# Optimization experiments

Measured on AMD Instinct MI355X. Metric: run time of the kernel, lower is better.

## Reference

```python
import jax, jax.numpy as jnp
import numpy as np
from jax import lax

B, V, E = 8, 1024, 32          # batch, nodes, raw node-embedding dim
F, H = 64, 4                   # node_encoding, num_heads
HID = 64                       # encoder/decoder hidden size
LAYERS = 2                     # graph_layers
FLOW_ITERS = 10
BIG = 1e9
COST_C = 1.0                   # quadratic cost: c*x^2, inv_derivative(y)=y/(2c)
DEG_P = 16.0 / V               # ~16 avg out-degree


def setup_inputs() -> dict:
    key = jax.random.key(0)
    ks = jax.random.split(key, 24)
    demands = jax.random.normal(ks[0], (B, V, 1), jnp.float32)
    demands = demands - jnp.mean(demands, axis=1, keepdims=True)  # balanced supply/demand
    node_embeddings = jax.random.normal(ks[1], (V, E), jnp.float32)
    adj = (jax.random.uniform(ks[2], (V, V)) < DEG_P).astype(jnp.float32)
    adj = jnp.maximum(adj, jnp.eye(V, dtype=jnp.float32))  # ensure nonempty rows
    s = 0.05
    p = lambda k, shp: jax.random.normal(k, shp, jnp.float32) * s
    return {
        'demands': demands, 'node_embeddings': node_embeddings, 'adj': adj,
        'enc_w1': p(ks[3], (E + 1, HID)), 'enc_b1': jnp.zeros((HID,), jnp.float32),
        'enc_w2': p(ks[4], (HID, F)),     'enc_b2': jnp.zeros((F,), jnp.float32),
        'gat_w':  p(ks[5], (H, F, F)),
        'gat_a1': p(ks[6], (H, F)), 'gat_a2': p(ks[7], (H, F)),
        'gate_w': p(ks[8], (F, F)), 'gate_u': p(ks[9], (F, F)),
        'gate_b': jnp.zeros((F,), jnp.float32),
        'dec_w1': p(ks[10], (F, HID)), 'dec_b1': jnp.zeros((HID,), jnp.float32),
        'dec_w2': p(ks[11], (HID, V)), 'dec_b2': jnp.zeros((V,), jnp.float32),
        'dual_w1': p(ks[12], (F, HID)), 'dual_b1': jnp.zeros((HID,), jnp.float32),
        'dual_w2': p(ks[13], (HID, 1)), 'dual_b2': jnp.zeros((1,), jnp.float32),
    }


def _forward(demands, node_embeddings, adj,
             enc_w1, enc_b1, enc_w2, enc_b2,
             gat_w, gat_a1, gat_a2,
             gate_w, gate_u, gate_b,
             dec_w1, dec_b1, dec_w2, dec_b2,
             dual_w1, dual_b1, dual_w2, dual_b2):
    node_bias = -BIG * (1.0 - adj)                     # [V, V]
    # ---- encoder MLP (relu hidden) ----
    x = jnp.broadcast_to(node_embeddings[None], (B, V, E))
    x = jnp.concatenate([x, demands], axis=2)          # [B, V, E+1]
    enc = jax.nn.relu(x @ enc_w1 + enc_b1) @ enc_w2 + enc_b2   # [B, V, F]
    enc = jax.nn.relu(enc)
    # ---- GAT + gate, shared weights across graph_layers ----
    for _ in range(LAYERS):
        t = jnp.einsum('bvf,hfg->bhvg', enc, gat_w)            # [B, H, V, F]
        s_self = jnp.einsum('bhvg,hg->bhv', t, gat_a1)
        s_nbr = jnp.einsum('bhvg,hg->bhv', t, gat_a2)
        logits = jax.nn.leaky_relu(s_self[..., :, None] + s_nbr[..., None, :], 0.2)
        coefs = jax.nn.softmax(logits + node_bias[None, None], axis=-1)  # [B,H,V,V]
        heads = jnp.einsum('bhvw,bhwg->bhvg', coefs, t)
        nxt = jax.nn.relu(jnp.mean(heads, axis=1))             # [B, V, F]
        z = jax.nn.sigmoid(nxt @ gate_w + enc @ gate_u + gate_b)
        enc = z * nxt + (1.0 - z) * enc
    # ---- decoder -> masked softmax flow weights ----
    pred = (enc @ dec_w1 + dec_b1) @ dec_w2 + dec_b2           # [B, V, V] (linear MLP)
    pred = jnp.square(pred)
    flow_weights = jax.nn.softmax(pred + node_bias[None], axis=-1)
    # ---- iterative min-cost-flow solve ----
    def flow_step(flow, _):
        inflow = jnp.sum(flow, axis=1)[:, :, None]             # [B, V, 1]
        return flow_weights * jax.nn.relu(inflow - demands), None
    flow, _ = lax.scan(flow_step, jnp.zeros_like(flow_weights), None, length=FLOW_ITERS)[0], None
    flow = lax.scan(flow_step, jnp.zeros_like(flow_weights), None, length=FLOW_ITERS)[0]
    flow_cost = jnp.sum(COST_C * jnp.square(flow), axis=(1, 2))  # [B]
    # ---- dual variables / dual cost ----
    dv = (enc @ dual_w1 + dual_b1) @ dual_w2 + dual_b2         # [B, V, 1]
    dual_diff = dv - jnp.swapaxes(dv, 1, 2)                    # [B, V, V]
    dual_flows = adj[None] * jax.nn.relu(dual_diff / (2.0 * COST_C))
    dual_flow_cost = COST_C * jnp.square(dual_flows) - dual_diff * dual_flows
    dual_demand = jnp.sum(dv * demands, axis=(1, 2))
    dual_cost = jnp.sum(dual_flow_cost, axis=(1, 2)) - dual_demand
    loss = jnp.mean(flow_cost - dual_cost)
    return loss


def reference(demands, node_embeddings, adj,
              enc_w1, enc_b1, enc_w2, enc_b2,
              gat_w, gat_a1, gat_a2,
              gate_w, gate_u, gate_b,
              dec_w1, dec_b1, dec_w2, dec_b2,
              dual_w1, dual_b1, dual_w2, dual_b2):
    return _forward(demands, node_embeddings, adj,
                    enc_w1, enc_b1, enc_w2, enc_b2,
                    gat_w, gat_a1, gat_a2,
                    gate_w, gate_u, gate_b,
                    dec_w1, dec_b1, dec_w2, dec_b2,
                    dual_w1, dual_b1, dual_w2, dual_b2)
```

## Files before the change

kernel.cpp:

```cpp
#include <hip/hip_runtime.h>
#include <math.h>

#define B 8
#define V 1024
#define E 32
#define H 4
#define HIDN 64
#define CAP 64
#define MAXNNZ 20480
#define SE (MAXNNZ / V)
#define ZBLK 128


__device__ __forceinline__ float wave_sum(float v) {
  for (int o = 32; o > 0; o >>= 1) v += __shfl_xor(v, o);
  return v;
}
__device__ __forceinline__ float wave_max(float v) {
  for (int o = 32; o > 0; o >>= 1) v = fmaxf(v, __shfl_xor(v, o));
  return v;
}

__global__ void zero_wa_kernel(int* __restrict__ deg_in, const float* __restrict__ gat_w,
                               const float* __restrict__ a1, const float* __restrict__ a2,
                               float* __restrict__ wa1, float* __restrict__ wa2) {
  if (blockIdx.x < 4) {
    deg_in[blockIdx.x * 256 + threadIdx.x] = 0;
  } else {
    int h = threadIdx.x >> 6, f = threadIdx.x & 63;
    float s1 = 0.f, s2 = 0.f;
    const float* W = gat_w + h * 4096 + f * 64;
    for (int g = 0; g < 64; ++g) {
      float w = W[g];
      s1 += w * a1[h * 64 + g];
      s2 += w * a2[h * 64 + g];
    }
    wa1[h * 64 + f] = s1;
    wa2[h * 64 + f] = s2;
  }
}

#define ENV 8
__global__ void setup_kernel(const float* __restrict__ adj, const float* __restrict__ demands,
                             const float* __restrict__ emb,
                             const float* __restrict__ ew1, const float* __restrict__ eb1,
                             const float* __restrict__ ew2, const float* __restrict__ eb2,
                             const float* __restrict__ dec_w2,
                             const float* __restrict__ wa1, const float* __restrict__ wa2,
                             int* __restrict__ nbr, int* __restrict__ deg,
                             int* __restrict__ deg_in, float* __restrict__ enc,
                             float* __restrict__ ss, float* __restrict__ sn,
                             float* __restrict__ w2t, float* __restrict__ fwe,
                             unsigned int* __restrict__ meta) {
  int blk = blockIdx.x;
  int j = threadIdx.x;
  if (blk < V) {
    int v = blk;
    int base = 0;
    for (int c = 0; c < V; c += 64) {
      float a = adj[v * V + c + j];
      unsigned long long m = __ballot(a > 0.5f);
      int pos = __popcll(m & ((1ull << j) - 1ull));
      if (a > 0.5f && base + pos < CAP) {
        nbr[v * CAP + base + pos] = c + j;
        atomicAdd(&deg_in[c + j], 1);
      }
      base += __popcll(m);
    }
    if (j == 0) deg[v] = (base < CAP) ? base : CAP;
  } else if (blk < 2 * V) {
    int eb = blk - V;
    int b = eb & 7;
    int v0 = (eb >> 3) * ENV;
    int bv0 = b * V + v0;
    __shared__ float xs[ENV][E + 1];
    __shared__ float hs[ENV][64];
#pragma unroll
    for (int n = 0; n < ENV; ++n) {
      if (j < E) xs[n][j] = emb[(v0 + n) * E + j];
      else if (j == E) xs[n][E] = demands[b * V + v0 + n];
    }
    __syncthreads();
    float h[ENV];
#pragma unroll
    for (int n = 0; n < ENV; ++n) h[n] = eb1[j];
    for (int i = 0; i < E + 1; ++i) {
      float wv = ew1[i * 64 + j];
#pragma unroll
      for (int n = 0; n < ENV; ++n) h[n] += xs[n][i] * wv;
    }
#pragma unroll
    for (int n = 0; n < ENV; ++n) hs[n][j] = fmaxf(h[n], 0.f);
    __syncthreads();
    float o[ENV];
#pragma unroll
    for (int n = 0; n < ENV; ++n) o[n] = eb2[j];
    for (int i = 0; i < 64; ++i) {
      float wv = ew2[i * 64 + j];
#pragma unroll
      for (int n = 0; n < ENV; ++n) o[n] += hs[n][i] * wv;
    }
#pragma unroll
    for (int n = 0; n < ENV; ++n) {
      o[n] = fmaxf(o[n], 0.f);
      enc[(bv0 + n) * 64 + j] = o[n];
    }
#pragma unroll
    for (int n = 0; n < ENV; ++n) {
#pragma unroll
      for (int hh = 0; hh < H; ++hh) {
        float v1 = wave_sum(o[n] * wa1[hh * 64 + j]);
        float v2 = wave_sum(o[n] * wa2[hh * 64 + j]);
        if (j == 0) {
          ss[(b * H + hh) * V + v0 + n] = v1;
          sn[(b * H + hh) * V + v0 + n] = v2;
        }
      }
    }
  } else if (blk < 3 * V) {
    int w = blk - 2 * V;
    w2t[w * 64 + j] = dec_w2[j * V + w];
  } else {
    int idx = (blk - 3 * V) * 64 + j;
    for (int i = idx; i < B * MAXNNZ; i += ZBLK * 64) fwe[i] = 0.f;
    for (int i = idx; i < MAXNNZ; i += ZBLK * 64) meta[i] = 0u;
  }
}

__global__ void scan_kernel(const int* __restrict__ deg_in, int* __restrict__ in_off) {
  int lane = threadIdx.x;
  int vals[16];
  int tot = 0;
#pragma unroll
  for (int i = 0; i < 16; ++i) {
    vals[i] = tot;
    tot += deg_in[lane * 16 + i];
  }
  int run = tot;
  for (int o = 1; o < 64; o <<= 1) {
    int u = __shfl_up(run, o);
    if (lane >= o) run += u;
  }
  int excl = run - tot;
#pragma unroll
  for (int i = 0; i < 16; ++i) in_off[lane * 16 + i] = excl + vals[i];
  if (lane == 63) in_off[V] = excl + tot;
}

__global__ void csc_fill(const int* __restrict__ nbr, const int* __restrict__ deg,
                         int* __restrict__ deg_in, const int* __restrict__ in_off,
                         int* __restrict__ csc_pos) {
  int v = blockIdx.x, k = threadIdx.x;
  if (k < deg[v]) {
    int w = nbr[v * CAP + k];
    int old = atomicSub(&deg_in[w], 1);
    csc_pos[v * CAP + k] = in_off[w] + old - 1;
  }
}

#define GNV 8
__global__ __launch_bounds__(256) void gat2_kernel(
    const float* __restrict__ enc_in, const float* __restrict__ ss_in,
    const float* __restrict__ sn_in, const int* __restrict__ nbr,
    const int* __restrict__ deg, const float* __restrict__ gat_w,
    const float* __restrict__ gate_w, const float* __restrict__ gate_u,
    const float* __restrict__ gate_b, const float* __restrict__ wa1,
    const float* __restrict__ wa2, float* __restrict__ enc_out,
    float* __restrict__ ss_out, float* __restrict__ sn_out, int write_s) {
  int b = blockIdx.x & 7;
  int v0 = (blockIdx.x >> 3) * GNV;
  int tid = threadIdx.x;
  int wid = tid >> 6, lane = tid & 63;
  __shared__ float agg[GNV][H][64];
  __shared__ float gpart[GNV][4][64];
  __shared__ float nxts[GNV][64];
  __shared__ float encs[GNV][64];
  const float* eb = enc_in + (size_t)b * V * 64;
  for (int i = tid; i < GNV * 64; i += 256) encs[i >> 6][i & 63] = eb[v0 * 64 + i];
  for (int n = wid; n < GNV; n += 4) {
    int v = v0 + n;
    int dvv = deg[v];
    int wk = (lane < dvv) ? nbr[v * CAP + lane] : 0;
    float c[H];
#pragma unroll
    for (int h = 0; h < H; ++h) {
      float x = ss_in[(b * H + h) * V + v] + sn_in[(b * H + h) * V + wk];
      x = (x > 0.f) ? x : 0.2f * x;
      if (lane >= dvv) x = -1e30f;
      float m = wave_max(x);
      float e = (lane < dvv) ? __expf(x - m) : 0.f;
      float s = wave_sum(e);
      c[h] = e / s;
    }
    float a0 = 0.f, a1v = 0.f, a2v = 0.f, a3v = 0.f;
    for (int k = 0; k < dvv; ++k) {
      int w = __shfl(wk, k);
      float ev = eb[w * 64 + lane];
      a0 += __shfl(c[0], k) * ev;
      a1v += __shfl(c[1], k) * ev;
      a2v += __shfl(c[2], k) * ev;
      a3v += __shfl(c[3], k) * ev;
    }
    agg[n][0][lane] = a0;
    agg[n][1][lane] = a1v;
    agg[n][2][lane] = a2v;
    agg[n][3][lane] = a3v;
  }
  __syncthreads();
  {
    const float* W = gat_w + wid * 4096;
    float hv[GNV];
#pragma unroll
    for (int n = 0; n < GNV; ++n) hv[n] = 0.f;
    for (int f = 0; f < 64; ++f) {
      float wf = W[f * 64 + lane];
#pragma unroll
      for (int n = 0; n < GNV; ++n) hv[n] += agg[n][wid][f] * wf;
    }
#pragma unroll
    for (int n = 0; n < GNV; ++n) gpart[n][wid][lane] = hv[n];
  }
  __syncthreads();
  for (int i = tid; i < GNV * 64; i += 256) {
    int n = i >> 6, g = i & 63;
    float s4 = gpart[n][0][g] + gpart[n][1][g] + gpart[n][2][g] + gpart[n][3][g];
    nxts[n][g] = fmaxf(0.25f * s4, 0.f);
  }
  __syncthreads();
  {
    float part[GNV];
#pragma unroll
    for (int n = 0; n < GNV; ++n) part[n] = 0.f;
    for (int f = wid * 16; f < wid * 16 + 16; ++f) {
      float gw = gate_w[f * 64 + lane], gu = gate_u[f * 64 + lane];
#pragma unroll
      for (int n = 0; n < GNV; ++n) part[n] += nxts[n][f] * gw + encs[n][f] * gu;
    }
    __syncthreads();
#pragma unroll
    for (int n = 0; n < GNV; ++n) gpart[n][wid][lane] = part[n];
  }
  __syncthreads();
  for (int i = tid; i < GNV * 64; i += 256) {
    int n = i >> 6, g = i & 63;
    float zs = gpart[n][0][g] + gpart[n][1][g] + gpart[n][2][g] + gpart[n][3][g] + gate_b[g];
    float z = 1.f / (1.f + __expf(-zs));
    float out = z * nxts[n][g] + (1.f - z) * encs[n][g];
    encs[n][g] = out;
    enc_out[((size_t)b * V + v0 + n) * 64 + g] = out;
  }
  if (write_s) {
    __syncthreads();
    float w1v = wa1[wid * 64 + lane], w2v = wa2[wid * 64 + lane];
#pragma unroll
    for (int n = 0; n < GNV; ++n) {
      float e = encs[n][lane];
      float ssv = wave_sum(e * w1v);
      float snv = wave_sum(e * w2v);
      if (lane == 0) {
        ss_out[(b * H + wid) * V + v0 + n] = ssv;
        sn_out[(b * H + wid) * V + v0 + n] = snv;
      }
    }
  }
}

#define DNV 8
__global__ void dec_dual_kernel(const float* __restrict__ enc, const float* __restrict__ dw1,
                                const float* __restrict__ db1, const float* __restrict__ uw1,
                                const float* __restrict__ ub1, const float* __restrict__ uw2,
                                const float* __restrict__ ub2, float* __restrict__ hid,
                                float* __restrict__ dv) {
  int b = blockIdx.x & 7;
  int v0 = (blockIdx.x >> 3) * DNV;
  int bv0 = b * V + v0;
  int j = threadIdx.x;
  __shared__ float es[DNV][64];
#pragma unroll
  for (int n = 0; n < DNV; ++n) es[n][j] = enc[(bv0 + n) * 64 + j];
  __syncthreads();
  float hj[DNV], uj[DNV];
#pragma unroll
  for (int n = 0; n < DNV; ++n) { hj[n] = db1[j]; uj[n] = ub1[j]; }
  for (int f = 0; f < 64; ++f) {
    float a = dw1[f * 64 + j], c = uw1[f * 64 + j];
#pragma unroll
    for (int n = 0; n < DNV; ++n) {
      hj[n] += es[n][f] * a;
      uj[n] += es[n][f] * c;
    }
  }
  float w2v = uw2[j];
#pragma unroll
  for (int n = 0; n < DNV; ++n) {
    hid[(bv0 + n) * 64 + j] = hj[n];
    float s = wave_sum(uj[n] * w2v);
    if (j == 0) dv[bv0 + n] = s + ub2[0];
  }
}

__global__ void fw_kernel(const float* __restrict__ hid, const float* __restrict__ w2t,
                          const float* __restrict__ b2, const int* __restrict__ nbr,
                          const int* __restrict__ deg, const int* __restrict__ csc_pos,
                          float* __restrict__ fwe, unsigned int* __restrict__ meta,
                          float* __restrict__ rssq) {
  int b = blockIdx.x & 7;
  int v = blockIdx.x >> 3;
  int bv = b * V + v;
  int k = threadIdx.x;
  __shared__ float hs[64];
  hs[k] = hid[bv * 64 + k];
  __syncthreads();
  int dvv = deg[v];
  int w = (k < dvv) ? nbr[v * CAP + k] : 0;
  const float4* wrow = (const float4*)(w2t + w * 64);
  const float4* hv4 = (const float4*)hs;
  float d = 0.f;
#pragma unroll
  for (int f = 0; f < 16; ++f) {
    float4 wv = wrow[f];
    float4 hv = hv4[f];
    d += hv.x * wv.x + hv.y * wv.y + hv.z * wv.z + hv.w * wv.w;
  }
  d += b2[w];
  float pp = d * d;
  float myp = (k < dvv) ? pp : -1e30f;
  float m = wave_max(myp);
  float e = (k < dvv) ? __expf(myp - m) : 0.f;
  float s = wave_sum(e);
  float coef = e / s;
  if (k < dvv) {
    int idx = csc_pos[v * CAP + k];
    fwe[(size_t)b * MAXNNZ + idx] = coef;
    meta[idx] = (unsigned)v | ((unsigned)w << 16);
  }
  float r = wave_sum(coef * coef);
  if (k == 0) rssq[bv] = r;
}

__global__ __launch_bounds__(1024) void flow_dual_kernel(
    const float* __restrict__ fwe, const unsigned int* __restrict__ meta,
    const float* __restrict__ rssq, const float* __restrict__ dv,
    const float* __restrict__ demands, const int* __restrict__ nbr_out,
    const int* __restrict__ deg_out, float* __restrict__ partial) {
  int b = blockIdx.x;
  int v = threadIdx.x;
  __shared__ float o[V], infl[V], dvs[V];
  __shared__ float red[16];
  float dem = demands[b * V + v];
  dvs[v] = dv[b * V + v];
  o[v] = fmaxf(-dem, 0.f);
  infl[v] = 0.f;
  const float4* fp = (const float4*)(fwe + (size_t)b * MAXNNZ + v * SE);
  const uint4* mp = (const uint4*)(meta + v * SE);
  float fr[SE];
  unsigned mr[SE];
#pragma unroll
  for (int i = 0; i < SE / 4; ++i) {
    float4 f4 = fp[i];
    uint4 m4 = mp[i];
    fr[4 * i + 0] = f4.x; fr[4 * i + 1] = f4.y; fr[4 * i + 2] = f4.z; fr[4 * i + 3] = f4.w;
    mr[4 * i + 0] = m4.x; mr[4 * i + 1] = m4.y; mr[4 * i + 2] = m4.z; mr[4 * i + 3] = m4.w;
  }
  __syncthreads();
  for (int it = 0; it < 9; ++it) {
    float acc = 0.f;
    int pdst = -1;
#pragma unroll
    for (int i = 0; i < SE; ++i) {
      int src = mr[i] & 0xFFFF;
      int dst = mr[i] >> 16;
      if (dst != pdst) {
        if (acc != 0.f) atomicAdd(&infl[pdst], acc);
        acc = 0.f;
        pdst = dst;
      }
      acc += fr[i] * o[src];
    }
    if (acc != 0.f) atomicAdd(&infl[pdst], acc);
    __syncthreads();
    float nv = fmaxf(infl[v] - dem, 0.f);
    o[v] = nv;
    infl[v] = 0.f;
    __syncthreads();
  }
  float o10 = o[v];
  float local = o10 * o10 * rssq[b * V + v];
  float dvv = dvs[v];
  int dout = deg_out[v];
  float acc = 0.f;
  for (int k = 0; k < dout; ++k) {
    float diff = dvv - dvs[nbr_out[v * CAP + k]];
    if (diff > 0.f) acc += diff * diff;
  }
  local += 0.25f * acc + dvv * dem;
  local = wave_sum(local);
  if ((v & 63) == 0) red[v >> 6] = local;
  __syncthreads();
  if (v < 16) {
    float r = red[v];
    for (int o2 = 8; o2 > 0; o2 >>= 1) r += __shfl_xor(r, o2, 16);
    if (v == 0) partial[b] = r;
  }
}

__global__ void final_kernel(const float* __restrict__ partial, float* __restrict__ out) {
  if (threadIdx.x == 0) {
    float s = 0.f;
    for (int b = 0; b < B; ++b) s += partial[b];
    out[0] = s * (1.0f / B);
  }
}

extern "C" void kernel_launch(void* const* d_in, const int* in_sizes, int n_in,
                              void* d_out, int out_size, void* d_ws, size_t ws_size,
                              hipStream_t stream) {
  const float* demands = (const float*)d_in[0];
  const float* emb     = (const float*)d_in[1];
  const float* adj     = (const float*)d_in[2];
  const float* enc_w1  = (const float*)d_in[3];
  const float* enc_b1  = (const float*)d_in[4];
  const float* enc_w2  = (const float*)d_in[5];
  const float* enc_b2  = (const float*)d_in[6];
  const float* gat_w   = (const float*)d_in[7];
  const float* gat_a1  = (const float*)d_in[8];
  const float* gat_a2  = (const float*)d_in[9];
  const float* gate_w  = (const float*)d_in[10];
  const float* gate_u  = (const float*)d_in[11];
  const float* gate_b  = (const float*)d_in[12];
  const float* dec_w1  = (const float*)d_in[13];
  const float* dec_b1  = (const float*)d_in[14];
  const float* dec_w2  = (const float*)d_in[15];
  const float* dec_b2  = (const float*)d_in[16];
  const float* dual_w1 = (const float*)d_in[17];
  const float* dual_b1 = (const float*)d_in[18];
  const float* dual_w2 = (const float*)d_in[19];
  const float* dual_b2 = (const float*)d_in[20];

  char* p = (char*)d_ws;
  auto alloc = [&](size_t n) { void* r = (void*)p; p += (n + 255) & ~(size_t)255; return r; };
  int* nbr_out   = (int*)alloc((size_t)V * CAP * 4);
  int* deg_out   = (int*)alloc((size_t)V * 4);
  int* deg_in    = (int*)alloc((size_t)V * 4);
  int* in_off    = (int*)alloc((size_t)(V + 1) * 4);
  int* csc_pos   = (int*)alloc((size_t)V * CAP * 4);
  float* fwe     = (float*)alloc((size_t)B * MAXNNZ * 4);
  unsigned int* meta = (unsigned int*)alloc((size_t)MAXNNZ * 4);
  float* w2t     = (float*)alloc((size_t)HIDN * V * 4);
  float* wa1     = (float*)alloc((size_t)H * 64 * 4);
  float* wa2     = (float*)alloc((size_t)H * 64 * 4);
  float* encA    = (float*)alloc((size_t)B * V * 64 * 4);
  float* encB    = (float*)alloc((size_t)B * V * 64 * 4);
  float* ssA     = (float*)alloc((size_t)B * H * V * 4);
  float* snA     = (float*)alloc((size_t)B * H * V * 4);
  float* ssB     = (float*)alloc((size_t)B * H * V * 4);
  float* snB     = (float*)alloc((size_t)B * H * V * 4);
  float* hid     = (float*)alloc((size_t)B * V * 64 * 4);
  float* dv      = (float*)alloc((size_t)B * V * 4);
  float* rssq    = (float*)alloc((size_t)B * V * 4);
  float* partial = (float*)alloc((size_t)B * 4);

  zero_wa_kernel<<<5, 256, 0, stream>>>(deg_in, gat_w, gat_a1, gat_a2, wa1, wa2);
  setup_kernel<<<3 * V + ZBLK, 64, 0, stream>>>(
      adj, demands, emb, enc_w1, enc_b1, enc_w2, enc_b2, dec_w2, wa1, wa2,
      nbr_out, deg_out, deg_in, encA, ssA, snA, w2t, fwe, meta);
  scan_kernel<<<1, 64, 0, stream>>>(deg_in, in_off);
  csc_fill<<<V, 64, 0, stream>>>(nbr_out, deg_out, deg_in, in_off, csc_pos);
  gat2_kernel<<<B * V / GNV, 256, 0, stream>>>(encA, ssA, snA, nbr_out, deg_out, gat_w,
                                               gate_w, gate_u, gate_b, wa1, wa2,
                                               encB, ssB, snB, 1);
  gat2_kernel<<<B * V / GNV, 256, 0, stream>>>(encB, ssB, snB, nbr_out, deg_out, gat_w,
                                               gate_w, gate_u, gate_b, wa1, wa2,
                                               encA, ssA, snA, 0);
  dec_dual_kernel<<<B * V / DNV, 64, 0, stream>>>(encA, dec_w1, dec_b1, dual_w1, dual_b1,
                                                  dual_w2, dual_b2, hid, dv);
  fw_kernel<<<B * V, 64, 0, stream>>>(hid, w2t, dec_b2, nbr_out, deg_out, csc_pos,
                                      fwe, meta, rssq);
  flow_dual_kernel<<<B, 1024, 0, stream>>>(fwe, meta, rssq, dv, demands, nbr_out, deg_out,
                                           partial);
  final_kernel<<<1, 64, 0, stream>>>(partial, (float*)d_out);
}
```

Measured before the change: 150.9 us.

## Fuse CSC build, decoder/fw and final reduction into neighbouring kernels

```diff
diff --git a/kernel.cpp b/kernel.cpp
--- a/kernel.cpp
+++ b/kernel.cpp
@@ -5,7 +5,6 @@
 #define V 1024
 #define E 32
 #define H 4
-#define HIDN 64
 #define CAP 64
 #define MAXNNZ 20480
 #define SE (MAXNNZ / V)
@@ -21,13 +20,18 @@
   return v;
 }
 
-__global__ void zero_wa_kernel(int* __restrict__ deg_in, const float* __restrict__ gat_w,
+__global__ void zero_wa_kernel(int* __restrict__ deg_in, int* __restrict__ slot_cur,
+                               unsigned* __restrict__ done, const float* __restrict__ gat_w,
                                const float* __restrict__ a1, const float* __restrict__ a2,
                                float* __restrict__ wa1, float* __restrict__ wa2) {
-  if (blockIdx.x < 4) {
-    deg_in[blockIdx.x * 256 + threadIdx.x] = 0;
+  int blk = blockIdx.x, tid = threadIdx.x;
+  if (blk < 4) {
+    deg_in[blk * 256 + tid] = 0;
+  } else if (blk < 8) {
+    slot_cur[(blk - 4) * 256 + tid] = 0;
   } else {
-    int h = threadIdx.x >> 6, f = threadIdx.x & 63;
+    if (tid == 0) *done = 0u;
+    int h = tid >> 6, f = tid & 63;
     float s1 = 0.f, s2 = 0.f;
     const float* W = gat_w + h * 4096 + f * 64;
     for (int g = 0; g < 64; ++g) {
@@ -127,37 +131,6 @@
   }
 }
 
-__global__ void scan_kernel(const int* __restrict__ deg_in, int* __restrict__ in_off) {
-  int lane = threadIdx.x;
-  int vals[16];
-  int tot = 0;
-#pragma unroll
-  for (int i = 0; i < 16; ++i) {
-    vals[i] = tot;
-    tot += deg_in[lane * 16 + i];
-  }
-  int run = tot;
-  for (int o = 1; o < 64; o <<= 1) {
-    int u = __shfl_up(run, o);
-    if (lane >= o) run += u;
-  }
-  int excl = run - tot;
-#pragma unroll
-  for (int i = 0; i < 16; ++i) in_off[lane * 16 + i] = excl + vals[i];
-  if (lane == 63) in_off[V] = excl + tot;
-}
-
-__global__ void csc_fill(const int* __restrict__ nbr, const int* __restrict__ deg,
-                         int* __restrict__ deg_in, const int* __restrict__ in_off,
-                         int* __restrict__ csc_pos) {
-  int v = blockIdx.x, k = threadIdx.x;
-  if (k < deg[v]) {
-    int w = nbr[v * CAP + k];
-    int old = atomicSub(&deg_in[w], 1);
-    csc_pos[v * CAP + k] = in_off[w] + old - 1;
-  }
-}
-
 #define GNV 8
 __global__ __launch_bounds__(256) void gat2_kernel(
     const float* __restrict__ enc_in, const float* __restrict__ ss_in,
@@ -166,7 +139,9 @@
     const float* __restrict__ gate_w, const float* __restrict__ gate_u,
     const float* __restrict__ gate_b, const float* __restrict__ wa1,
     const float* __restrict__ wa2, float* __restrict__ enc_out,
-    float* __restrict__ ss_out, float* __restrict__ sn_out, int write_s) {
+    float* __restrict__ ss_out, float* __restrict__ sn_out, int write_s,
+    const int* __restrict__ deg_in, int* __restrict__ slot_cur,
+    int* __restrict__ csc_pos, int do_csc) {
   int b = blockIdx.x & 7;
   int v0 = (blockIdx.x >> 3) * GNV;
   int tid = threadIdx.x;
@@ -175,6 +150,7 @@
   __shared__ float gpart[GNV][4][64];
   __shared__ float nxts[GNV][64];
   __shared__ float encs[GNV][64];
+  __shared__ int ioff[V];
   const float* eb = enc_in + (size_t)b * V * 64;
   for (int i = tid; i < GNV * 64; i += 256) encs[i >> 6][i & 63] = eb[v0 * 64 + i];
   for (int n = wid; n < GNV; n += 4) {
@@ -263,86 +239,98 @@
       }
     }
   }
-}
-
-#define DNV 8
-__global__ void dec_dual_kernel(const float* __restrict__ enc, const float* __restrict__ dw1,
-                                const float* __restrict__ db1, const float* __restrict__ uw1,
-                                const float* __restrict__ ub1, const float* __restrict__ uw2,
-                                const float* __restrict__ ub2, float* __restrict__ hid,
-                                float* __restrict__ dv) {
+  if (do_csc && b == 0) {
+    __syncthreads();
+    if (tid < 64) {
+      int vals[16];
+      int tot = 0;
+#pragma unroll
+      for (int i = 0; i < 16; ++i) {
+        vals[i] = tot;
+        tot += deg_in[tid * 16 + i];
+      }
+      int run = tot;
+      for (int o = 1; o < 64; o <<= 1) {
+        int u = __shfl_up(run, o);
+        if (lane >= o) run += u;
+      }
+      int excl = run - tot;
+#pragma unroll
+      for (int i = 0; i < 16; ++i) ioff[tid * 16 + i] = excl + vals[i];
+    }
+    __syncthreads();
+    for (int n = wid; n < GNV; n += 4) {
+      int v = v0 + n;
+      if (lane < deg[v]) {
+        int w = nbr[v * CAP + lane];
+        csc_pos[v * CAP + lane] = ioff[w] + atomicAdd(&slot_cur[w], 1);
+      }
+    }
+  }
+}
+
+#define DNV 4
+__global__ __launch_bounds__(256) void decfw_kernel(
+    const float* __restrict__ enc, const float* __restrict__ dw1,
+    const float* __restrict__ db1, const float* __restrict__ uw1,
+    const float* __restrict__ ub1, const float* __restrict__ uw2,
+    const float* __restrict__ ub2, const float* __restrict__ w2t,
+    const float* __restrict__ dec_b2, const int* __restrict__ nbr,
+    const int* __restrict__ deg, const int* __restrict__ csc_pos,
+    float* __restrict__ fwe, unsigned int* __restrict__ meta,
+    float* __restrict__ rssq, float* __restrict__ dvout) {
   int b = blockIdx.x & 7;
   int v0 = (blockIdx.x >> 3) * DNV;
   int bv0 = b * V + v0;
-  int j = threadIdx.x;
+  int tid = threadIdx.x;
+  int wv = tid >> 6, j = tid & 63;
   __shared__ float es[DNV][64];
-#pragma unroll
-  for (int n = 0; n < DNV; ++n) es[n][j] = enc[(bv0 + n) * 64 + j];
-  __syncthreads();
-  float hj[DNV], uj[DNV];
-#pragma unroll
-  for (int n = 0; n < DNV; ++n) { hj[n] = db1[j]; uj[n] = ub1[j]; }
+  __shared__ float hs[DNV][64];
+  es[wv][j] = enc[(bv0 + wv) * 64 + j];
+  __syncthreads();
+  float hj = db1[j], uj = ub1[j];
   for (int f = 0; f < 64; ++f) {
-    float a = dw1[f * 64 + j], c = uw1[f * 64 + j];
-#pragma unroll
-    for (int n = 0; n < DNV; ++n) {
-      hj[n] += es[n][f] * a;
-      uj[n] += es[n][f] * c;
-    }
-  }
-  float w2v = uw2[j];
-#pragma unroll
-  for (int n = 0; n < DNV; ++n) {
-    hid[(bv0 + n) * 64 + j] = hj[n];
-    float s = wave_sum(uj[n] * w2v);
-    if (j == 0) dv[bv0 + n] = s + ub2[0];
-  }
-}
-
-__global__ void fw_kernel(const float* __restrict__ hid, const float* __restrict__ w2t,
-                          const float* __restrict__ b2, const int* __restrict__ nbr,
-                          const int* __restrict__ deg, const int* __restrict__ csc_pos,
-                          float* __restrict__ fwe, unsigned int* __restrict__ meta,
-                          float* __restrict__ rssq) {
-  int b = blockIdx.x & 7;
-  int v = blockIdx.x >> 3;
-  int bv = b * V + v;
-  int k = threadIdx.x;
-  __shared__ float hs[64];
-  hs[k] = hid[bv * 64 + k];
-  __syncthreads();
+    hj += es[wv][f] * dw1[f * 64 + j];
+    uj += es[wv][f] * uw1[f * 64 + j];
+  }
+  hs[wv][j] = hj;
+  float sdv = wave_sum(uj * uw2[j]);
+  if (j == 0) dvout[bv0 + wv] = sdv + ub2[0];
+  __syncthreads();
+  int v = v0 + wv;
   int dvv = deg[v];
-  int w = (k < dvv) ? nbr[v * CAP + k] : 0;
+  int w = (j < dvv) ? nbr[v * CAP + j] : 0;
   const float4* wrow = (const float4*)(w2t + w * 64);
-  const float4* hv4 = (const float4*)hs;
+  const float4* hv4 = (const float4*)hs[wv];
   float d = 0.f;
 #pragma unroll
   for (int f = 0; f < 16; ++f) {
-    float4 wv = wrow[f];
+    float4 wvv = wrow[f];
     float4 hv = hv4[f];
-    d += hv.x * wv.x + hv.y * wv.y + hv.z * wv.z + hv.w * wv.w;
-  }
-  d += b2[w];
+    d += hv.x * wvv.x + hv.y * wvv.y + hv.z * wvv.z + hv.w * wvv.w;
+  }
+  d += dec_b2[w];
   float pp = d * d;
-  float myp = (k < dvv) ? pp : -1e30f;
+  float myp = (j < dvv) ? pp : -1e30f;
   float m = wave_max(myp);
-  float e = (k < dvv) ? __expf(myp - m) : 0.f;
+  float e = (j < dvv) ? __expf(myp - m) : 0.f;
   float s = wave_sum(e);
   float coef = e / s;
-  if (k < dvv) {
-    int idx = csc_pos[v * CAP + k];
+  if (j < dvv) {
+    int idx = csc_pos[v * CAP + j];
     fwe[(size_t)b * MAXNNZ + idx] = coef;
     meta[idx] = (unsigned)v | ((unsigned)w << 16);
   }
   float r = wave_sum(coef * coef);
-  if (k == 0) rssq[bv] = r;
+  if (j == 0) rssq[bv0 + wv] = r;
 }
 
 __global__ __launch_bounds__(1024) void flow_dual_kernel(
-    const float* __restrict__ fwe, const unsigned int* __restrict__ meta,
+    const float* __restrict__ fwe, const unsigned* __restrict__ meta,
     const float* __restrict__ rssq, const float* __restrict__ dv,
     const float* __restrict__ demands, const int* __restrict__ nbr_out,
-    const int* __restrict__ deg_out, float* __restrict__ partial) {
+    const int* __restrict__ deg_out, float* __restrict__ partial,
+    unsigned* __restrict__ done, float* __restrict__ out) {
   int b = blockIdx.x;
   int v = threadIdx.x;
   __shared__ float o[V], infl[V], dvs[V];
@@ -400,15 +388,16 @@
   if (v < 16) {
     float r = red[v];
     for (int o2 = 8; o2 > 0; o2 >>= 1) r += __shfl_xor(r, o2, 16);
-    if (v == 0) partial[b] = r;
-  }
-}
-
-__global__ void final_kernel(const float* __restrict__ partial, float* __restrict__ out) {
-  if (threadIdx.x == 0) {
-    float s = 0.f;
-    for (int b = 0; b < B; ++b) s += partial[b];
-    out[0] = s * (1.0f / B);
+    if (v == 0) {
+      __hip_atomic_store(&partial[b], r, __ATOMIC_RELEASE, __HIP_MEMORY_SCOPE_AGENT);
+      unsigned old = __hip_atomic_fetch_add(done, 1u, __ATOMIC_ACQ_REL, __HIP_MEMORY_SCOPE_AGENT);
+      if (old == B - 1) {
+        float s = 0.f;
+        for (int i = 0; i < B; ++i)
+          s += __hip_atomic_load(&partial[i], __ATOMIC_ACQUIRE, __HIP_MEMORY_SCOPE_AGENT);
+        out[0] = s * (1.0f / B);
+      }
+    }
   }
 }
 
@@ -437,16 +426,18 @@
   const float* dual_w2 = (const float*)d_in[19];
   const float* dual_b2 = (const float*)d_in[20];
 
-  char* p = (char*)d_ws;
+  char* pz = (char*)d_ws;
+  int* deg_in   = (int*)pz;
+  int* slot_cur = (int*)(pz + 4096);
+  unsigned* done = (unsigned*)(pz + 8192);
+  char* p = pz + 8448;
   auto alloc = [&](size_t n) { void* r = (void*)p; p += (n + 255) & ~(size_t)255; return r; };
   int* nbr_out   = (int*)alloc((size_t)V * CAP * 4);
   int* deg_out   = (int*)alloc((size_t)V * 4);
-  int* deg_in    = (int*)alloc((size_t)V * 4);
-  int* in_off    = (int*)alloc((size_t)(V + 1) * 4);
   int* csc_pos   = (int*)alloc((size_t)V * CAP * 4);
   float* fwe     = (float*)alloc((size_t)B * MAXNNZ * 4);
   unsigned int* meta = (unsigned int*)alloc((size_t)MAXNNZ * 4);
-  float* w2t     = (float*)alloc((size_t)HIDN * V * 4);
+  float* w2t     = (float*)alloc((size_t)64 * V * 4);
   float* wa1     = (float*)alloc((size_t)H * 64 * 4);
   float* wa2     = (float*)alloc((size_t)H * 64 * 4);
   float* encA    = (float*)alloc((size_t)B * V * 64 * 4);
@@ -455,28 +446,26 @@
   float* snA     = (float*)alloc((size_t)B * H * V * 4);
   float* ssB     = (float*)alloc((size_t)B * H * V * 4);
   float* snB     = (float*)alloc((size_t)B * H * V * 4);
-  float* hid     = (float*)alloc((size_t)B * V * 64 * 4);
   float* dv      = (float*)alloc((size_t)B * V * 4);
   float* rssq    = (float*)alloc((size_t)B * V * 4);
   float* partial = (float*)alloc((size_t)B * 4);
 
-  zero_wa_kernel<<<5, 256, 0, stream>>>(deg_in, gat_w, gat_a1, gat_a2, wa1, wa2);
+  zero_wa_kernel<<<9, 256, 0, stream>>>(deg_in, slot_cur, done, gat_w, gat_a1, gat_a2,
+                                        wa1, wa2);
   setup_kernel<<<3 * V + ZBLK, 64, 0, stream>>>(
       adj, demands, emb, enc_w1, enc_b1, enc_w2, enc_b2, dec_w2, wa1, wa2,
       nbr_out, deg_out, deg_in, encA, ssA, snA, w2t, fwe, meta);
-  scan_kernel<<<1, 64, 0, stream>>>(deg_in, in_off);
-  csc_fill<<<V, 64, 0, stream>>>(nbr_out, deg_out, deg_in, in_off, csc_pos);
   gat2_kernel<<<B * V / GNV, 256, 0, stream>>>(encA, ssA, snA, nbr_out, deg_out, gat_w,
                                                gate_w, gate_u, gate_b, wa1, wa2,
-                                               encB, ssB, snB, 1);
+                                               encB, ssB, snB, 1,
+                                               deg_in, slot_cur, csc_pos, 1);
   gat2_kernel<<<B * V / GNV, 256, 0, stream>>>(encB, ssB, snB, nbr_out, deg_out, gat_w,
                                                gate_w, gate_u, gate_b, wa1, wa2,
-                                               encA, ssA, snA, 0);
-  dec_dual_kernel<<<B * V / DNV, 64, 0, stream>>>(encA, dec_w1, dec_b1, dual_w1, dual_b1,
-                                                  dual_w2, dual_b2, hid, dv);
-  fw_kernel<<<B * V, 64, 0, stream>>>(hid, w2t, dec_b2, nbr_out, deg_out, csc_pos,
-                                      fwe, meta, rssq);
+                                               encA, ssA, snA, 0,
+                                               deg_in, slot_cur, csc_pos, 0);
+  decfw_kernel<<<B * V / DNV, 256, 0, stream>>>(encA, dec_w1, dec_b1, dual_w1, dual_b1,
+                                                dual_w2, dual_b2, w2t, dec_b2, nbr_out,
+                                                deg_out, csc_pos, fwe, meta, rssq, dv);
   flow_dual_kernel<<<B, 1024, 0, stream>>>(fwe, meta, rssq, dv, demands, nbr_out, deg_out,
-                                           partial);
-  final_kernel<<<1, 64, 0, stream>>>(partial, (float*)d_out);
-}
+                                           partial, done, (float*)d_out);
+}
```

Result: faster. 147.9 us (-2.0%).
